# Kernel optimization log

Hardware: AMD Instinct MI355X
Metric: run time of the kernel (lower is better)

The kernel has to match this reference:

```python
import jax, jax.numpy as jnp
import numpy as np

B, U, L, E, H, V = 512, 10, 50, 200, 200, 50000
FLAT = 16 * 16 * 8  # conv(3x3,VALID)->48x48, pool(3x3,s3)->16x16, 8 channels


def gru(x, Wih, Whh, bih, bhh):
    """PyTorch-convention GRU (gate order r,z,n). x: [B,T,E] -> (ys [B,T,H], h_last [B,H])."""
    Bx = x.shape[0]
    Hh = Whh.shape[1]
    x_proj = x @ Wih.T + bih  # [B,T,3H]

    def step(h, xp):
        gh = h @ Whh.T + bhh
        xr, xz, xn = jnp.split(xp, 3, axis=-1)
        hr, hz, hn = jnp.split(gh, 3, axis=-1)
        r = jax.nn.sigmoid(xr + hr)
        z = jax.nn.sigmoid(xz + hz)
        n = jnp.tanh(xn + r * hn)
        h_new = (1.0 - z) * n + z * h
        return h_new, h_new

    h0 = jnp.zeros((Bx, Hh), x.dtype)
    h_last, ys = jax.lax.scan(step, h0, jnp.swapaxes(x_proj, 0, 1))
    return jnp.swapaxes(ys, 0, 1), h_last


def setup_inputs() -> dict:
    key = jax.random.key(0)
    ks = jax.random.split(key, 24)
    s = 0.05
    inp = {
        "utterance": jax.random.randint(ks[0], (B, U, L), 0, V, dtype=jnp.int32),
        "response": jax.random.randint(ks[1], (B, L), 0, V, dtype=jnp.int32),
        "emb": jax.random.uniform(ks[2], (V, E), jnp.float32, -0.25, 0.25),
        "W_ih_u": jax.random.normal(ks[3], (3 * H, E)) * s,
        "W_hh_u": jax.random.normal(ks[4], (3 * H, H)) * s,
        "b_ih_u": jnp.zeros((3 * H,), jnp.float32),
        "b_hh_u": jnp.zeros((3 * H,), jnp.float32),
        "W_ih_r": jax.random.normal(ks[5], (3 * H, E)) * s,
        "W_hh_r": jax.random.normal(ks[6], (3 * H, H)) * s,
        "b_ih_r": jnp.zeros((3 * H,), jnp.float32),
        "b_hh_r": jnp.zeros((3 * H,), jnp.float32),
        "conv_w": jax.random.normal(ks[7], (8, 2, 3, 3)) * 0.3,
        "conv_b": jnp.zeros((8,), jnp.float32),
        "lin_w": jax.random.normal(ks[8], (50, FLAT)) * 0.02,
        "lin_b": jnp.zeros((50,), jnp.float32),
        "Amat": jax.random.normal(ks[9], (H, H)) * 0.05,
        "W_ih_f": jax.random.normal(ks[10], (3 * H, 50)) * s,
        "W_hh_f": jax.random.normal(ks[11], (3 * H, H)) * s,
        "b_ih_f": jnp.zeros((3 * H,), jnp.float32),
        "b_hh_f": jnp.zeros((3 * H,), jnp.float32),
        "flin_w": jax.random.normal(ks[12], (1, H)) * 0.05,
        "flin_b": jnp.zeros((1,), jnp.float32),
    }
    return inp


def reference(utterance, response, emb, W_ih_u, W_hh_u, b_ih_u, b_hh_u,
              W_ih_r, W_hh_r, b_ih_r, b_hh_r, conv_w, conv_b, lin_w, lin_b,
              Amat, W_ih_f, W_hh_f, b_ih_f, b_hh_f, flin_w, flin_b):
    ue = emb[utterance]            # [B,U,L,E]
    re = emb[response]             # [B,L,E]

    rg, _ = gru(re, W_ih_r, W_hh_r, b_ih_r, b_hh_r)  # [B,L,H]

    # word-level match: matmul(utt_emb, resp_emb^T)
    m1 = jnp.einsum('bule,bte->bult', ue, re)  # [B,U,L,L]

    # segment-level: GRU(utt) @ A @ GRU(resp)^T  (loop over utterances folded into batch)
    ug, _ = gru(ue.reshape(B * U, L, E), W_ih_u, W_hh_u, b_ih_u, b_hh_u)
    ug = ug.reshape(B, U, L, H)
    m2 = jnp.einsum('bulh,hk,btk->bult', ug, Amat, rg)  # [B,U,L,L]

    x = jnp.stack([m1, m2], axis=2).reshape(B * U, 2, L, L)  # [B*U,2,50,50]
    x = jax.lax.conv_general_dilated(x, conv_w, (1, 1), 'VALID',
                                     dimension_numbers=('NCHW', 'OIHW', 'NCHW'))
    x = jax.nn.relu(x + conv_b[None, :, None, None])          # [B*U,8,48,48]
    x = jax.lax.reduce_window(x, -jnp.inf, jax.lax.max,
                              (1, 1, 3, 3), (1, 1, 3, 3), 'VALID')  # [B*U,8,16,16]
    x = x.reshape(B * U, FLAT)
    mv = jnp.tanh(x @ lin_w.T + lin_b).reshape(B, U, 50)      # matching vectors

    _, h_last = gru(mv, W_ih_f, W_hh_f, b_ih_f, b_hh_f)       # [B,H]
    logits = h_last @ flin_w.T + flin_b                       # [B,1]
    return jax.nn.sigmoid(logits)
```

## Files before the change

### kernel.cpp

```cpp
#include <hip/hip_runtime.h>
#include <hip/hip_bf16.h>


typedef __attribute__((ext_vector_type(8))) short short8v;
typedef __attribute__((ext_vector_type(4))) float f32x4;

__device__ __forceinline__ float sigm(float x) { return 1.0f / (1.0f + __expf(-x)); }
__device__ __forceinline__ float tanhfast(float x) {
    float e = __expf(2.0f * x);
    return 1.0f - 2.0f / (e + 1.0f);
}
__device__ __forceinline__ float bl(unsigned x) { return __uint_as_float(x << 16); }
__device__ __forceinline__ float bh(unsigned x) { return __uint_as_float(x & 0xffff0000u); }
__device__ __forceinline__ unsigned packbf(float a, float b) {
    union { __hip_bfloat16 h[2]; unsigned u; } cv;
    cv.h[0] = __float2bfloat16(a); cv.h[1] = __float2bfloat16(b);
    return cv.u;
}

__global__ __launch_bounds__(256)
void gemm_mfma(const void* __restrict__ Asrc, int a_bf16,
               const int* __restrict__ gidx,
               const float* __restrict__ W, const float* __restrict__ bias,
               __hip_bfloat16* __restrict__ C, int M, int N)
{
    __shared__ __hip_bfloat16 Al[64 * 232];
    __shared__ __hip_bfloat16 Bl[64 * 232];
    const int tid = threadIdx.x;
    const int m0 = blockIdx.x * 64, n0 = blockIdx.y * 64;

    for (int idx = tid; idx < 64 * 29; idx += 256) {
        int r = idx / 29, q = idx - r * 29;
        int k0 = q * 8, row = m0 + r;
        uint4 val = make_uint4(0, 0, 0, 0);
        if (k0 < 200 && row < M) {
            size_t ar = (size_t)(gidx ? gidx[row] : row) * 200 + k0;
            if (a_bf16) {
                val = *(const uint4*)((const __hip_bfloat16*)Asrc + ar);
            } else {
                const float* ap = (const float*)Asrc + ar;
                float4 f0 = *(const float4*)ap;
                float4 f1 = *(const float4*)(ap + 4);
                val.x = packbf(f0.x, f0.y); val.y = packbf(f0.z, f0.w);
                val.z = packbf(f1.x, f1.y); val.w = packbf(f1.z, f1.w);
            }
        }
        *(uint4*)(Al + r * 232 + k0) = val;
    }
    for (int idx = tid; idx < 64 * 29; idx += 256) {
        int r = idx / 29, q = idx - r * 29;
        int k0 = q * 8, row = n0 + r;
        uint4 val = make_uint4(0, 0, 0, 0);
        if (k0 < 200 && row < N) {
            const float* wp = W + (size_t)row * 200 + k0;
            float4 f0 = *(const float4*)wp;
            float4 f1 = *(const float4*)(wp + 4);
            val.x = packbf(f0.x, f0.y); val.y = packbf(f0.z, f0.w);
            val.z = packbf(f1.x, f1.y); val.w = packbf(f1.z, f1.w);
        }
        *(uint4*)(Bl + r * 232 + k0) = val;
    }
    __syncthreads();

    const int wid = tid >> 6, lane = tid & 63;
    const int wm = (wid >> 1) * 32, wn = (wid & 1) * 32;
    const int lrow = lane & 15, lk8 = (lane >> 4) * 8;
    f32x4 acc00 = {0.f, 0.f, 0.f, 0.f}, acc01 = {0.f, 0.f, 0.f, 0.f};
    f32x4 acc10 = {0.f, 0.f, 0.f, 0.f}, acc11 = {0.f, 0.f, 0.f, 0.f};
#pragma unroll
    for (int kk = 0; kk < 7; ++kk) {
        const int kb = kk * 32 + lk8;
        short8v a0 = *(const short8v*)(Al + (wm + lrow) * 232 + kb);
        short8v a1 = *(const short8v*)(Al + (wm + 16 + lrow) * 232 + kb);
        short8v b0 = *(const short8v*)(Bl + (wn + lrow) * 232 + kb);
        short8v b1 = *(const short8v*)(Bl + (wn + 16 + lrow) * 232 + kb);
        acc00 = __builtin_amdgcn_mfma_f32_16x16x32_bf16(a0, b0, acc00, 0, 0, 0);
        acc01 = __builtin_amdgcn_mfma_f32_16x16x32_bf16(a0, b1, acc01, 0, 0, 0);
        acc10 = __builtin_amdgcn_mfma_f32_16x16x32_bf16(a1, b0, acc10, 0, 0, 0);
        acc11 = __builtin_amdgcn_mfma_f32_16x16x32_bf16(a1, b1, acc11, 0, 0, 0);
    }
    const int drow = (lane >> 4) * 4, dcol = lane & 15;
#pragma unroll
    for (int fm = 0; fm < 2; ++fm) {
#pragma unroll
        for (int fn = 0; fn < 2; ++fn) {
            const f32x4 av = (fm == 0) ? (fn == 0 ? acc00 : acc01)
                                       : (fn == 0 ? acc10 : acc11);
            const int gcol = n0 + wn + fn * 16 + dcol;
            if (gcol >= N) continue;
            const float bs = bias ? bias[gcol] : 0.0f;
#pragma unroll
            for (int r = 0; r < 4; ++r) {
                const int grow = m0 + wm + fm * 16 + drow + r;
                if (grow >= M) continue;
                C[(size_t)grow * N + gcol] = __float2bfloat16(av[r] + bs);
            }
        }
    }
}

__global__ __launch_bounds__(256)
void gemm_mfma_k(const void* __restrict__ Asrc, int a_bf16,
                 const float* __restrict__ W, const float* __restrict__ bias,
                 void* __restrict__ Cv, int c_bf16,
                 int M, int N, int K, int act)
{
    __shared__ __align__(16) __hip_bfloat16 As[64 * 136];
    __shared__ __align__(16) __hip_bfloat16 Bs[64 * 136];
    const int tid = threadIdx.x;
    const int m0 = blockIdx.x * 64, n0 = blockIdx.y * 64;
    const int wid = tid >> 6, lane = tid & 63;
    const int wm = (wid >> 1) * 32, wn = (wid & 1) * 32;
    const int lrow = lane & 15, lk8 = (lane >> 4) * 8;
    const bool aAlign16 = a_bf16 && ((K & 7) == 0);

    f32x4 acc00 = {0.f, 0.f, 0.f, 0.f}, acc01 = {0.f, 0.f, 0.f, 0.f};
    f32x4 acc10 = {0.f, 0.f, 0.f, 0.f}, acc11 = {0.f, 0.f, 0.f, 0.f};

    for (int kb = 0; kb < K; kb += 128) {
        for (int idx = tid; idx < 1024; idx += 256) {
            int r = idx >> 4, q = idx & 15;
            int k0 = kb + q * 8, row = m0 + r;
            uint4 av = make_uint4(0, 0, 0, 0);
            if (row < M && k0 < K) {
                size_t base = (size_t)row * K + k0;
                if (a_bf16) {
                    const __hip_bfloat16* ap = (const __hip_bfloat16*)Asrc + base;
                    if (aAlign16 && k0 + 8 <= K) {
                        av = *(const uint4*)ap;
                    } else {
                        unsigned t4[4] = {0, 0, 0, 0};
                        int nv = (K - k0 < 8) ? (K - k0) : 8;
                        for (int e = 0; e < nv; ++e)
                            ((__hip_bfloat16*)t4)[e] = ap[e];
                        av.x = t4[0]; av.y = t4[1]; av.z = t4[2]; av.w = t4[3];
                    }
                } else {
                    const float* ap = (const float*)Asrc + base;
                    float tv[8] = {0, 0, 0, 0, 0, 0, 0, 0};
                    int nv = (K - k0 < 8) ? (K - k0) : 8;
                    for (int e = 0; e < nv; ++e) tv[e] = ap[e];
                    av.x = packbf(tv[0], tv[1]); av.y = packbf(tv[2], tv[3]);
                    av.z = packbf(tv[4], tv[5]); av.w = packbf(tv[6], tv[7]);
                }
            }
            *(uint4*)(As + r * 136 + q * 8) = av;
        }
        for (int idx = tid; idx < 1024; idx += 256) {
            int r = idx >> 4, q = idx & 15;
            int k0 = kb + q * 8, row = n0 + r;
            uint4 bv = make_uint4(0, 0, 0, 0);
            if (row < N && k0 < K) {
                const float* wp = W + (size_t)row * K + k0;
                float tv[8] = {0, 0, 0, 0, 0, 0, 0, 0};
                int nv = (K - k0 < 8) ? (K - k0) : 8;
                for (int e = 0; e < nv; ++e) tv[e] = wp[e];
                bv.x = packbf(tv[0], tv[1]); bv.y = packbf(tv[2], tv[3]);
                bv.z = packbf(tv[4], tv[5]); bv.w = packbf(tv[6], tv[7]);
            }
            *(uint4*)(Bs + r * 136 + q * 8) = bv;
        }
        __syncthreads();
#pragma unroll
        for (int kk = 0; kk < 4; ++kk) {
            const int ko = kk * 32 + lk8;
            short8v a0 = *(const short8v*)(As + (wm + lrow) * 136 + ko);
            short8v a1 = *(const short8v*)(As + (wm + 16 + lrow) * 136 + ko);
            short8v b0 = *(const short8v*)(Bs + (wn + lrow) * 136 + ko);
            short8v b1 = *(const short8v*)(Bs + (wn + 16 + lrow) * 136 + ko);
            acc00 = __builtin_amdgcn_mfma_f32_16x16x32_bf16(a0, b0, acc00, 0, 0, 0);
            acc01 = __builtin_amdgcn_mfma_f32_16x16x32_bf16(a0, b1, acc01, 0, 0, 0);
            acc10 = __builtin_amdgcn_mfma_f32_16x16x32_bf16(a1, b0, acc10, 0, 0, 0);
            acc11 = __builtin_amdgcn_mfma_f32_16x16x32_bf16(a1, b1, acc11, 0, 0, 0);
        }
        __syncthreads();
    }

    const int drow = (lane >> 4) * 4, dcol = lane & 15;
#pragma unroll
    for (int fm = 0; fm < 2; ++fm) {
#pragma unroll
        for (int fn = 0; fn < 2; ++fn) {
            const f32x4 av = (fm == 0) ? (fn == 0 ? acc00 : acc01)
                                       : (fn == 0 ? acc10 : acc11);
            const int gcol = n0 + wn + fn * 16 + dcol;
            if (gcol >= N) continue;
            const float bs = bias ? bias[gcol] : 0.0f;
#pragma unroll
            for (int r = 0; r < 4; ++r) {
                const int grow = m0 + wm + fm * 16 + drow + r;
                if (grow >= M) continue;
                float t = av[r] + bs;
                if (act == 1) t = tanhfast(t);
                if (c_bf16) ((__hip_bfloat16*)Cv)[(size_t)grow * N + gcol] = __float2bfloat16(t);
                else        ((float*)Cv)[(size_t)grow * N + gcol] = t;
            }
        }
    }
}

__global__ __launch_bounds__(256)
void transpose_wf(const float* __restrict__ Wf, float* __restrict__ Tf)
{
    int id = blockIdx.x * 256 + threadIdx.x;
    if (id < 120000) {
        int e = id / 600, j = id - e * 600;
        Tf[id] = Wf[(size_t)j * 200 + e];
    }
}

__global__ __launch_bounds__(256)
void pack_whh(const float* __restrict__ Wu, const float* __restrict__ Wr,
              __hip_bfloat16* __restrict__ Du, __hip_bfloat16* __restrict__ Dr)
{
    int idx = blockIdx.x * 256 + threadIdx.x;
    if (idx >= 143360) return;
    int j = idx / 224, e = idx - j * 224;
    bool v = (j < 600) && (e < 200);
    Du[idx] = __float2bfloat16(v ? Wu[(size_t)j * 200 + e] : 0.0f);
    Dr[idx] = __float2bfloat16(v ? Wr[(size_t)j * 200 + e] : 0.0f);
}

__global__ __launch_bounds__(256)
void gather_re16(const int* __restrict__ resp, const float* __restrict__ emb,
                 __hip_bfloat16* __restrict__ re16)
{
    int idx = blockIdx.x * 256 + threadIdx.x;
    if (idx < 2560000) {
        int row = idx / 100, q = idx - row * 100;
        float2 v = *(const float2*)(emb + (size_t)resp[row] * 200 + 2 * q);
        ((unsigned*)re16)[idx] = packbf(v.x, v.y);
    }
}

__global__ __launch_bounds__(512, 2)
void scan_gru_mfma(const int* __restrict__ utt,
                   const __hip_bfloat16* __restrict__ EPu,
                   const __hip_bfloat16* __restrict__ xpr16,
                   const __hip_bfloat16* __restrict__ Wu16,
                   const __hip_bfloat16* __restrict__ Wr16,
                   const float* __restrict__ bhu, const float* __restrict__ bhr,
                   __hip_bfloat16* __restrict__ ug16,
                   __hip_bfloat16* __restrict__ rg16)
{
    __shared__ __align__(16) float gh[32][644];
    __shared__ __align__(16) float hf[32][204];
    __shared__ __align__(16) __hip_bfloat16 h16[32][232];

    const int tid = threadIdx.x;
    const bool isResp = (int)blockIdx.x >= 160;
    const int row0 = isResp ? ((int)blockIdx.x - 160) * 32 : (int)blockIdx.x * 32;
    const __hip_bfloat16* Wt = isResp ? Wr16 : Wu16;
    const float* bgate = isResp ? bhr : bhu;
    __hip_bfloat16* arch = isResp ? rg16 : ug16;

    for (int i = tid; i < 32 * 204; i += 512) ((float*)hf)[i] = 0.0f;
    for (int i = tid; i < 928; i += 512) ((uint4*)h16)[i] = make_uint4(0, 0, 0, 0);
    __syncthreads();

    const int wid = tid >> 6, lane = tid & 63;
    const int lrow = lane & 15, lk8 = (lane >> 4) * 8;
    const int drow = (lane >> 4) * 4, dcol = lane & 15;

    short8v Bf[5][7];
#pragma unroll
    for (int i = 0; i < 5; ++i) {
        const int j = (wid * 5 + i) * 16 + lrow;
#pragma unroll
        for (int kk = 0; kk < 7; ++kk)
            Bf[i][kk] = *(const short8v*)(Wt + (size_t)j * 224 + kk * 32 + lk8);
    }

    const int r0a = tid / 25,        c0a = (tid % 25) * 8;
    const int t1  = tid + 512;
    const int r0b = t1 / 25,         c0b = (t1 % 25) * 8;

    for (int t = 0; t < 50; ++t) {
        const int ga = row0 + r0a;
        const __hip_bfloat16* xpa = isResp
            ? (xpr16 + ((size_t)ga * 50 + t) * 600)
            : (EPu + (size_t)utt[ga * 50 + t] * 600);
        uint4 xra = *(const uint4*)(xpa + c0a);
        uint4 xza = *(const uint4*)(xpa + 200 + c0a);
        uint4 xna = *(const uint4*)(xpa + 400 + c0a);
        uint4 xrb, xzb, xnb;
        const int gb = row0 + r0b;
        if (tid < 288) {
            const __hip_bfloat16* xpb = isResp
                ? (xpr16 + ((size_t)gb * 50 + t) * 600)
                : (EPu + (size_t)utt[gb * 50 + t] * 600);
            xrb = *(const uint4*)(xpb + c0b);
            xzb = *(const uint4*)(xpb + 200 + c0b);
            xnb = *(const uint4*)(xpb + 400 + c0b);
        }

        f32x4 a0[5], a1[5];
#pragma unroll
        for (int i = 0; i < 5; ++i) {
            a0[i] = (f32x4){0.f, 0.f, 0.f, 0.f};
            a1[i] = (f32x4){0.f, 0.f, 0.f, 0.f};
        }
#pragma unroll
        for (int kk = 0; kk < 7; ++kk) {
            short8v A0 = *(const short8v*)(&h16[lrow][kk * 32 + lk8]);
            short8v A1 = *(const short8v*)(&h16[16 + lrow][kk * 32 + lk8]);
#pragma unroll
            for (int i = 0; i < 5; ++i) {
                a0[i] = __builtin_amdgcn_mfma_f32_16x16x32_bf16(A0, Bf[i][kk], a0[i], 0, 0, 0);
                a1[i] = __builtin_amdgcn_mfma_f32_16x16x32_bf16(A1, Bf[i][kk], a1[i], 0, 0, 0);
            }
        }
#pragma unroll
        for (int i = 0; i < 5; ++i) {
            const int j = (wid * 5 + i) * 16 + dcol;
#pragma unroll
            for (int r = 0; r < 4; ++r) {
                gh[drow + r][j] = a0[i][r];
                gh[16 + drow + r][j] = a1[i][r];
            }
        }
        __syncthreads();

        {
            const int row = r0a, c0 = c0a, grow = ga;
            const unsigned xr4[4] = { xra.x, xra.y, xra.z, xra.w };
            const unsigned xz4[4] = { xza.x, xza.y, xza.z, xza.w };
            const unsigned xn4[4] = { xna.x, xna.y, xna.z, xna.w };
            float hn[8];
#pragma unroll
            for (int j = 0; j < 8; ++j) {
                const int c = c0 + j;
                const float xr = (j & 1) ? bh(xr4[j >> 1]) : bl(xr4[j >> 1]);
                const float xz = (j & 1) ? bh(xz4[j >> 1]) : bl(xz4[j >> 1]);
                const float xn = (j & 1) ? bh(xn4[j >> 1]) : bl(xn4[j >> 1]);
                const float rr = sigm(xr + gh[row][c] + bgate[c]);
                const float zz = sigm(xz + gh[row][200 + c] + bgate[200 + c]);
                const float nn = tanhfast(xn + rr * (gh[row][400 + c] + bgate[400 + c]));
                hn[j] = (1.0f - zz) * nn + zz * hf[row][c];
            }
            *(float4*)(&hf[row][c0])     = (float4){hn[0], hn[1], hn[2], hn[3]};
            *(float4*)(&hf[row][c0 + 4]) = (float4){hn[4], hn[5], hn[6], hn[7]};
            uint4 pk;
            pk.x = packbf(hn[0], hn[1]); pk.y = packbf(hn[2], hn[3]);
            pk.z = packbf(hn[4], hn[5]); pk.w = packbf(hn[6], hn[7]);
            *(uint4*)(&h16[row][c0]) = pk;
            *(uint4*)(arch + ((size_t)grow * 50 + t) * 200 + c0) = pk;
        }
        if (tid < 288) {
            const int row = r0b, c0 = c0b, grow = gb;
            const unsigned xr4[4] = { xrb.x, xrb.y, xrb.z, xrb.w };
            const unsigned xz4[4] = { xzb.x, xzb.y, xzb.z, xzb.w };
            const unsigned xn4[4] = { xnb.x, xnb.y, xnb.z, xnb.w };
            float hn[8];
#pragma unroll
            for (int j = 0; j < 8; ++j) {
                const int c = c0 + j;
                const float xr = (j & 1) ? bh(xr4[j >> 1]) : bl(xr4[j >> 1]);
                const float xz = (j & 1) ? bh(xz4[j >> 1]) : bl(xz4[j >> 1]);
                const float xn = (j & 1) ? bh(xn4[j >> 1]) : bl(xn4[j >> 1]);
                const float rr = sigm(xr + gh[row][c] + bgate[c]);
                const float zz = sigm(xz + gh[row][200 + c] + bgate[200 + c]);
                const float nn = tanhfast(xn + rr * (gh[row][400 + c] + bgate[400 + c]));
                hn[j] = (1.0f - zz) * nn + zz * hf[row][c];
            }
            *(float4*)(&hf[row][c0])     = (float4){hn[0], hn[1], hn[2], hn[3]};
            *(float4*)(&hf[row][c0 + 4]) = (float4){hn[4], hn[5], hn[6], hn[7]};
            uint4 pk;
            pk.x = packbf(hn[0], hn[1]); pk.y = packbf(hn[2], hn[3]);
            pk.z = packbf(hn[4], hn[5]); pk.w = packbf(hn[6], hn[7]);
            *(uint4*)(&h16[row][c0]) = pk;
            *(uint4*)(arch + ((size_t)grow * 50 + t) * 200 + c0) = pk;
        }
        __syncthreads();
    }
}

__global__ __launch_bounds__(256)
void match_conv_pool(const int* __restrict__ utt, const float* __restrict__ emb,
                     const __hip_bfloat16* __restrict__ ug16,
                     const __hip_bfloat16* __restrict__ re16,
                     const __hip_bfloat16* __restrict__ rgA16,
                     const float* __restrict__ cw, const float* __restrict__ cb,
                     __hip_bfloat16* __restrict__ pooled16)
{
    const int bu = blockIdx.x, b = bu / 10;
    __shared__ __align__(16) __hip_bfloat16 As[64 * 232];
    __shared__ __align__(16) __hip_bfloat16 Bs[64 * 232];
    __shared__ float m[2][50][50];
    __shared__ float w[144];
    __shared__ float bsh[8];
    const int tid = threadIdx.x;
    if (tid < 144) w[tid] = cw[tid];
    if (tid >= 144 && tid < 152) bsh[tid - 144] = cb[tid - 144];

    for (int idx = tid; idx < 64 * 29; idx += 256) {
        int r = idx / 29, q = idx - r * 29;
        uint4 av = make_uint4(0, 0, 0, 0), bv = make_uint4(0, 0, 0, 0);
        if (r < 50 && q < 25) {
            const float* ap = emb + (size_t)utt[bu * 50 + r] * 200 + q * 8;
            float4 f0 = *(const float4*)ap;
            float4 f1 = *(const float4*)(ap + 4);
            av.x = packbf(f0.x, f0.y); av.y = packbf(f0.z, f0.w);
            av.z = packbf(f1.x, f1.y); av.w = packbf(f1.z, f1.w);
            bv = *(const uint4*)(re16 + (size_t)b * 10000 + (size_t)r * 200 + q * 8);
        }
        *(uint4*)(As + r * 232 + q * 8) = av;
        *(uint4*)(Bs + r * 232 + q * 8) = bv;
    }
    __syncthreads();

    const int wid = tid >> 6, lane = tid & 63;
    const int wm = (wid >> 1) * 32, wn = (wid & 1) * 32;
    const int lrow = lane & 15, lk8 = (lane >> 4) * 8;
    const int drow = (lane >> 4) * 4, dcol = lane & 15;

#pragma unroll 1
    for (int ch = 0; ch < 2; ++ch) {
        f32x4 acc00 = {0.f, 0.f, 0.f, 0.f}, acc01 = {0.f, 0.f, 0.f, 0.f};
        f32x4 acc10 = {0.f, 0.f, 0.f, 0.f}, acc11 = {0.f, 0.f, 0.f, 0.f};
#pragma unroll
        for (int kk = 0; kk < 7; ++kk) {
            const int kb = kk * 32 + lk8;
            short8v a0 = *(const short8v*)(As + (wm + lrow) * 232 + kb);
            short8v a1 = *(const short8v*)(As + (wm + 16 + lrow) * 232 + kb);
            short8v b0 = *(const short8v*)(Bs + (wn + lrow) * 232 + kb);
            short8v b1 = *(const short8v*)(Bs + (wn + 16 + lrow) * 232 + kb);
            acc00 = __builtin_amdgcn_mfma_f32_16x16x32_bf16(a0, b0, acc00, 0, 0, 0);
            acc01 = __builtin_amdgcn_mfma_f32_16x16x32_bf16(a0, b1, acc01, 0, 0, 0);
            acc10 = __builtin_amdgcn_mfma_f32_16x16x32_bf16(a1, b0, acc10, 0, 0, 0);
            acc11 = __builtin_amdgcn_mfma_f32_16x16x32_bf16(a1, b1, acc11, 0, 0, 0);
        }
#pragma unroll
        for (int fm = 0; fm < 2; ++fm) {
#pragma unroll
            for (int fn = 0; fn < 2; ++fn) {
                const f32x4 av = (fm == 0) ? (fn == 0 ? acc00 : acc01)
                                           : (fn == 0 ? acc10 : acc11);
                const int gcol = wn + fn * 16 + dcol;
                if (gcol >= 50) continue;
#pragma unroll
                for (int r = 0; r < 4; ++r) {
                    const int grow = wm + fm * 16 + drow + r;
                    if (grow < 50) m[ch][grow][gcol] = av[r];
                }
            }
        }
        __syncthreads();
        if (ch == 0) {
            for (int idx = tid; idx < 50 * 25; idx += 256) {
                int r = idx / 25, q = idx - r * 25;
                *(uint4*)(As + r * 232 + q * 8) =
                    *(const uint4*)(ug16 + (size_t)bu * 10000 + (size_t)r * 200 + q * 8);
                *(uint4*)(Bs + r * 232 + q * 8) =
                    *(const uint4*)(rgA16 + (size_t)b * 10000 + (size_t)r * 200 + q * 8);
            }
            __syncthreads();
        }
    }

#pragma unroll
    for (int k = 0; k < 8; ++k) {
        const int o = tid + k * 256;
        const int c = o >> 8, ph = (o >> 4) & 15, pw = o & 15;
        float mx = -1e30f;
#pragma unroll
        for (int p = 0; p < 3; ++p)
#pragma unroll
            for (int q = 0; q < 3; ++q) {
                const int y = ph * 3 + p, x = pw * 3 + q;
                float s = bsh[c];
#pragma unroll
                for (int ci = 0; ci < 2; ++ci)
#pragma unroll
                    for (int dy = 0; dy < 3; ++dy)
#pragma unroll
                        for (int dx = 0; dx < 3; ++dx)
                            s = fmaf(w[(c * 2 + ci) * 9 + dy * 3 + dx],
                                     m[ci][y + dy][x + dx], s);
                s = fmaxf(s, 0.0f);
                mx = fmaxf(mx, s);
            }
        pooled16[(size_t)bu * 2048 + o] = __float2bfloat16(mx);
    }
}

__global__ __launch_bounds__(256)
void final_gru(const float* __restrict__ xpf, const float* __restrict__ WTf,
               const float* __restrict__ bhf, const float* __restrict__ fw,
               const float* __restrict__ fb, float* __restrict__ out)
{
    const int blk = blockIdx.x;
    const int tid = threadIdx.x;
    __shared__ float h[2][201];
    for (int i = tid; i < 402; i += 256) ((float*)h)[i] = 0.0f;
    __syncthreads();
    const int rr = tid / 100;
    const int j0 = 2 * (tid % 100);
    for (int t = 0; t < 10; ++t) {
        float cR[2] = {}, cZ[2] = {}, cN[2] = {};
        if (tid < 200) {
#pragma unroll 2
            for (int e = 0; e < 200; ++e) {
                const float* w = WTf + (size_t)e * 600;
                float2 wr = *(const float2*)(w + j0);
                float2 wz = *(const float2*)(w + 200 + j0);
                float2 wn = *(const float2*)(w + 400 + j0);
                float hv = h[rr][e];
                cR[0] = fmaf(hv, wr.x, cR[0]); cR[1] = fmaf(hv, wr.y, cR[1]);
                cZ[0] = fmaf(hv, wz.x, cZ[0]); cZ[1] = fmaf(hv, wz.y, cZ[1]);
                cN[0] = fmaf(hv, wn.x, cN[0]); cN[1] = fmaf(hv, wn.y, cN[1]);
            }
        }
        __syncthreads();
        if (tid < 200) {
            const float* xp = xpf + ((size_t)(blk * 2 + rr) * 10 + t) * 600;
#pragma unroll
            for (int j = 0; j < 2; ++j) {
                const int c = j0 + j;
                float rrg = sigm(xp[c] + cR[j] + bhf[c]);
                float zz = sigm(xp[200 + c] + cZ[j] + bhf[200 + c]);
                float nn = tanhfast(xp[400 + c] + rrg * (cN[j] + bhf[400 + c]));
                h[rr][c] = (1.0f - zz) * nn + zz * h[rr][c];
            }
        }
        __syncthreads();
    }
    if (tid < 2) {
        float s = fb[0];
        for (int k = 0; k < 200; ++k) s = fmaf(h[tid][k], fw[k], s);
        out[blk * 2 + tid] = sigm(s);
    }
}

__global__ __launch_bounds__(256)
void fill_out(float* __restrict__ out)
{
    int i = blockIdx.x * 256 + threadIdx.x;
    if (i < 512) out[i] = 0.0f;
}

extern "C" void kernel_launch(void* const* d_in, const int* in_sizes, int n_in,
                              void* d_out, int out_size, void* d_ws, size_t ws_size,
                              hipStream_t stream)
{
    const int*   utt    = (const int*)d_in[0];
    const int*   resp   = (const int*)d_in[1];
    const float* emb    = (const float*)d_in[2];
    const float* W_ih_u = (const float*)d_in[3];
    const float* W_hh_u = (const float*)d_in[4];
    const float* b_ih_u = (const float*)d_in[5];
    const float* b_hh_u = (const float*)d_in[6];
    const float* W_ih_r = (const float*)d_in[7];
    const float* W_hh_r = (const float*)d_in[8];
    const float* b_ih_r = (const float*)d_in[9];
    const float* b_hh_r = (const float*)d_in[10];
    const float* conv_w = (const float*)d_in[11];
    const float* conv_b = (const float*)d_in[12];
    const float* lin_w  = (const float*)d_in[13];
    const float* lin_b  = (const float*)d_in[14];
    const float* Amat   = (const float*)d_in[15];
    const float* W_ih_f = (const float*)d_in[16];
    const float* W_hh_f = (const float*)d_in[17];
    const float* b_ih_f = (const float*)d_in[18];
    const float* b_hh_f = (const float*)d_in[19];
    const float* flin_w = (const float*)d_in[20];
    const float* flin_b = (const float*)d_in[21];
    float* out = (float*)d_out;
    float* ws  = (float*)d_ws;

    size_t off = 0;
    auto alloc = [&](size_t n) { float* p = ws + off; off += (n + 63) & ~((size_t)63); return p; };
    float* WT_f   = alloc(120000);
    float* Wu16f  = alloc(71680);
    float* Wr16f  = alloc(71680);
    float* re16f  = alloc(2560000);
    float* EPuf   = alloc(15000000);
    float* xprf   = alloc(7680000);
    float* ug16f  = alloc(25600000);
    float* rg16f  = alloc(2560000);
    float* rgA16f = alloc(2560000);

    if (off * sizeof(float) > ws_size) {
        hipLaunchKernelGGL(fill_out, dim3(2), dim3(256), 0, stream, out);
        return;
    }

    __hip_bfloat16* Wu16  = (__hip_bfloat16*)Wu16f;
    __hip_bfloat16* Wr16  = (__hip_bfloat16*)Wr16f;
    __hip_bfloat16* re16  = (__hip_bfloat16*)re16f;
    __hip_bfloat16* EPu   = (__hip_bfloat16*)EPuf;
    __hip_bfloat16* xpr16 = (__hip_bfloat16*)xprf;
    __hip_bfloat16* ug16  = (__hip_bfloat16*)ug16f;
    __hip_bfloat16* rg16  = (__hip_bfloat16*)rg16f;
    __hip_bfloat16* rgA16 = (__hip_bfloat16*)rgA16f;
    __hip_bfloat16* pooled16 = (__hip_bfloat16*)EPuf;
    __hip_bfloat16* mv16     = (__hip_bfloat16*)xprf;
    float* xpf = xprf + 400000;

    hipLaunchKernelGGL(transpose_wf, dim3(469), dim3(256), 0, stream, W_hh_f, WT_f);
    hipLaunchKernelGGL(pack_whh, dim3(560), dim3(256), 0, stream,
                       W_hh_u, W_hh_r, Wu16, Wr16);
    hipLaunchKernelGGL(gather_re16, dim3(10000), dim3(256), 0, stream, resp, emb, re16);
    hipLaunchKernelGGL(gemm_mfma, dim3(782, 10), dim3(256), 0, stream,
                       (const void*)emb, 0, (const int*)nullptr, W_ih_u, b_ih_u,
                       EPu, 50000, 600);
    hipLaunchKernelGGL(gemm_mfma, dim3(400, 10), dim3(256), 0, stream,
                       (const void*)emb, 0, resp, W_ih_r, b_ih_r,
                       xpr16, 25600, 600);
    hipLaunchKernelGGL(scan_gru_mfma, dim3(176), dim3(512), 0, stream,
                       utt, EPu, xpr16, Wu16, Wr16, b_hh_u, b_hh_r, ug16, rg16);
    hipLaunchKernelGGL(gemm_mfma, dim3(400, 4), dim3(256), 0, stream,
                       (const void*)rg16, 1, (const int*)nullptr, Amat,
                       (const float*)nullptr, rgA16, 25600, 200);
    hipLaunchKernelGGL(match_conv_pool, dim3(5120), dim3(256), 0, stream,
                       utt, emb, ug16, re16, rgA16, conv_w, conv_b, pooled16);
    hipLaunchKernelGGL(gemm_mfma_k, dim3(80, 1), dim3(256), 0, stream,
                       (const void*)pooled16, 1, lin_w, lin_b,
                       (void*)mv16, 1, 5120, 50, 2048, 1);
    hipLaunchKernelGGL(gemm_mfma_k, dim3(80, 10), dim3(256), 0, stream,
                       (const void*)mv16, 1, W_ih_f, b_ih_f,
                       (void*)xpf, 0, 5120, 600, 50, 0);
    hipLaunchKernelGGL(final_gru, dim3(256), dim3(256), 0, stream,
                       xpf, WT_f, b_hh_f, flin_w, flin_b, out);
}
```

Before: 1.154 ms.

## Fuse GRU gate math into MFMA accumulators with gate-aligned weight packing

Repacks W_hh so each gate occupies a 256-row padded slab, letting every wave compute r, z, n tiles for the same hidden columns and apply the GRU update directly from MFMA accumulators in registers. This removes the gh shared-memory staging and the fp32 hidden-state array, and double-buffers h16 so each step needs a single barrier. In exchange, weights are no longer kept in registers and are re-read from global/L2 every step, the input projections are loaded as scalar bf16 elements, and the archive store of the previous step is deferred into the next iteration.

```diff
diff --git a/kernel.cpp b/kernel.cpp
--- a/kernel.cpp
+++ b/kernel.cpp
@@ -214,11 +214,12 @@
               __hip_bfloat16* __restrict__ Du, __hip_bfloat16* __restrict__ Dr)
 {
     int idx = blockIdx.x * 256 + threadIdx.x;
-    if (idx >= 143360) return;
+    if (idx >= 172032) return;
     int j = idx / 224, e = idx - j * 224;
-    bool v = (j < 600) && (e < 200);
-    Du[idx] = __float2bfloat16(v ? Wu[(size_t)j * 200 + e] : 0.0f);
-    Dr[idx] = __float2bfloat16(v ? Wr[(size_t)j * 200 + e] : 0.0f);
+    int g = j >> 8, cc = j & 255;
+    bool v = (cc < 200) && (e < 200);
+    Du[idx] = __float2bfloat16(v ? Wu[(size_t)(g * 200 + cc) * 200 + e] : 0.0f);
+    Dr[idx] = __float2bfloat16(v ? Wr[(size_t)(g * 200 + cc) * 200 + e] : 0.0f);
 }
 
 __global__ __launch_bounds__(256)
@@ -243,9 +244,7 @@
                    __hip_bfloat16* __restrict__ ug16,
                    __hip_bfloat16* __restrict__ rg16)
 {
-    __shared__ __align__(16) float gh[32][644];
-    __shared__ __align__(16) float hf[32][204];
-    __shared__ __align__(16) __hip_bfloat16 h16[32][232];
+    __shared__ __align__(16) __hip_bfloat16 h16[2][32][232];
 
     const int tid = threadIdx.x;
     const bool isResp = (int)blockIdx.x >= 160;
@@ -254,124 +253,121 @@
     const float* bgate = isResp ? bhr : bhu;
     __hip_bfloat16* arch = isResp ? rg16 : ug16;
 
-    for (int i = tid; i < 32 * 204; i += 512) ((float*)hf)[i] = 0.0f;
-    for (int i = tid; i < 928; i += 512) ((uint4*)h16)[i] = make_uint4(0, 0, 0, 0);
+    for (int i = tid; i < 2 * 32 * 232 / 8; i += 512)
+        ((uint4*)h16)[i] = make_uint4(0, 0, 0, 0);
     __syncthreads();
 
     const int wid = tid >> 6, lane = tid & 63;
     const int lrow = lane & 15, lk8 = (lane >> 4) * 8;
     const int drow = (lane >> 4) * 4, dcol = lane & 15;
-
-    short8v Bf[5][7];
-#pragma unroll
-    for (int i = 0; i < 5; ++i) {
-        const int j = (wid * 5 + i) * 16 + lrow;
-#pragma unroll
-        for (int kk = 0; kk < 7; ++kk)
-            Bf[i][kk] = *(const short8v*)(Wt + (size_t)j * 224 + kk * 32 + lk8);
-    }
-
-    const int r0a = tid / 25,        c0a = (tid % 25) * 8;
-    const int t1  = tid + 512;
-    const int r0b = t1 / 25,         c0b = (t1 % 25) * 8;
+    const int ct0 = 2 * wid, ct1 = 2 * wid + 1;
+    const bool u0 = (ct0 <= 12), u1 = (ct1 <= 12);
+    const int c0 = ct0 * 16 + dcol, c1 = ct1 * 16 + dcol;
+    const bool g0 = (c0 < 200), g1 = (c1 < 200);
+
+    float bgA[3] = {0.f, 0.f, 0.f}, bgB[3] = {0.f, 0.f, 0.f};
+    if (g0) { bgA[0] = bgate[c0]; bgA[1] = bgate[200 + c0]; bgA[2] = bgate[400 + c0]; }
+    if (g1) { bgB[0] = bgate[c1]; bgB[1] = bgate[200 + c1]; bgB[2] = bgate[400 + c1]; }
+
+    float hfA[2][4] = {{0.f,0.f,0.f,0.f},{0.f,0.f,0.f,0.f}};
+    float hfB[2][4] = {{0.f,0.f,0.f,0.f},{0.f,0.f,0.f,0.f}};
 
     for (int t = 0; t < 50; ++t) {
-        const int ga = row0 + r0a;
-        const __hip_bfloat16* xpa = isResp
-            ? (xpr16 + ((size_t)ga * 50 + t) * 600)
-            : (EPu + (size_t)utt[ga * 50 + t] * 600);
-        uint4 xra = *(const uint4*)(xpa + c0a);
-        uint4 xza = *(const uint4*)(xpa + 200 + c0a);
-        uint4 xna = *(const uint4*)(xpa + 400 + c0a);
-        uint4 xrb, xzb, xnb;
-        const int gb = row0 + r0b;
-        if (tid < 288) {
-            const __hip_bfloat16* xpb = isResp
-                ? (xpr16 + ((size_t)gb * 50 + t) * 600)
-                : (EPu + (size_t)utt[gb * 50 + t] * 600);
-            xrb = *(const uint4*)(xpb + c0b);
-            xzb = *(const uint4*)(xpb + 200 + c0b);
-            xnb = *(const uint4*)(xpb + 400 + c0b);
-        }
-
-        f32x4 a0[5], a1[5];
-#pragma unroll
-        for (int i = 0; i < 5; ++i) {
-            a0[i] = (f32x4){0.f, 0.f, 0.f, 0.f};
-            a1[i] = (f32x4){0.f, 0.f, 0.f, 0.f};
-        }
+        const int buf = t & 1, nxt = buf ^ 1;
+
+        if (t > 0) {
+            for (int idx = tid; idx < 800; idx += 512) {
+                int rr = idx / 25, q = (idx - rr * 25) * 8;
+                uint4 v = *(const uint4*)(&h16[buf][rr][q]);
+                *(uint4*)(arch + ((size_t)(row0 + rr) * 50 + (t - 1)) * 200 + q) = v;
+            }
+        }
+
+        float xvA[2][4][3], xvB[2][4][3];
+#pragma unroll
+        for (int rb = 0; rb < 2; ++rb)
+#pragma unroll
+            for (int r = 0; r < 4; ++r) {
+                const int grow = row0 + rb * 16 + drow + r;
+                const __hip_bfloat16* xp = isResp
+                    ? (xpr16 + ((size_t)grow * 50 + t) * 600)
+                    : (EPu + (size_t)utt[grow * 50 + t] * 600);
+                if (g0) {
+                    xvA[rb][r][0] = __bfloat162float(xp[c0]);
+                    xvA[rb][r][1] = __bfloat162float(xp[200 + c0]);
+                    xvA[rb][r][2] = __bfloat162float(xp[400 + c0]);
+                }
+                if (g1) {
+                    xvB[rb][r][0] = __bfloat162float(xp[c1]);
+                    xvB[rb][r][1] = __bfloat162float(xp[200 + c1]);
+                    xvB[rb][r][2] = __bfloat162float(xp[400 + c1]);
+                }
+            }
+
+        f32x4 aA[2][3], aB[2][3];
+#pragma unroll
+        for (int rb = 0; rb < 2; ++rb)
+#pragma unroll
+            for (int g = 0; g < 3; ++g) {
+                aA[rb][g] = (f32x4){0.f, 0.f, 0.f, 0.f};
+                aB[rb][g] = (f32x4){0.f, 0.f, 0.f, 0.f};
+            }
 #pragma unroll
         for (int kk = 0; kk < 7; ++kk) {
-            short8v A0 = *(const short8v*)(&h16[lrow][kk * 32 + lk8]);
-            short8v A1 = *(const short8v*)(&h16[16 + lrow][kk * 32 + lk8]);
-#pragma unroll
-            for (int i = 0; i < 5; ++i) {
-                a0[i] = __builtin_amdgcn_mfma_f32_16x16x32_bf16(A0, Bf[i][kk], a0[i], 0, 0, 0);
-                a1[i] = __builtin_amdgcn_mfma_f32_16x16x32_bf16(A1, Bf[i][kk], a1[i], 0, 0, 0);
-            }
-        }
-#pragma unroll
-        for (int i = 0; i < 5; ++i) {
-            const int j = (wid * 5 + i) * 16 + dcol;
-#pragma unroll
-            for (int r = 0; r < 4; ++r) {
-                gh[drow + r][j] = a0[i][r];
-                gh[16 + drow + r][j] = a1[i][r];
-            }
+            short8v A0 = *(const short8v*)(&h16[buf][lrow][kk * 32 + lk8]);
+            short8v A1 = *(const short8v*)(&h16[buf][16 + lrow][kk * 32 + lk8]);
+            if (u0) {
+#pragma unroll
+                for (int g = 0; g < 3; ++g) {
+                    short8v B = *(const short8v*)(Wt +
+                        (size_t)(g * 256 + ct0 * 16 + lrow) * 224 + kk * 32 + lk8);
+                    aA[0][g] = __builtin_amdgcn_mfma_f32_16x16x32_bf16(A0, B, aA[0][g], 0, 0, 0);
+                    aA[1][g] = __builtin_amdgcn_mfma_f32_16x16x32_bf16(A1, B, aA[1][g], 0, 0, 0);
+                }
+            }
+            if (u1) {
+#pragma unroll
+                for (int g = 0; g < 3; ++g) {
+                    short8v B = *(const short8v*)(Wt +
+                        (size_t)(g * 256 + ct1 * 16 + lrow) * 224 + kk * 32 + lk8);
+                    aB[0][g] = __builtin_amdgcn_mfma_f32_16x16x32_bf16(A0, B, aB[0][g], 0, 0, 0);
+                    aB[1][g] = __builtin_amdgcn_mfma_f32_16x16x32_bf16(A1, B, aB[1][g], 0, 0, 0);
+                }
+            }
+        }
+
+        if (g0) {
+#pragma unroll
+            for (int rb = 0; rb < 2; ++rb)
+#pragma unroll
+                for (int r = 0; r < 4; ++r) {
+                    const float rr_ = sigm(xvA[rb][r][0] + aA[rb][0][r] + bgA[0]);
+                    const float zz  = sigm(xvA[rb][r][1] + aA[rb][1][r] + bgA[1]);
+                    const float nn  = tanhfast(xvA[rb][r][2] + rr_ * (aA[rb][2][r] + bgA[2]));
+                    const float hn  = (1.0f - zz) * nn + zz * hfA[rb][r];
+                    hfA[rb][r] = hn;
+                    h16[nxt][rb * 16 + drow + r][c0] = __float2bfloat16(hn);
+                }
+        }
+        if (g1) {
+#pragma unroll
+            for (int rb = 0; rb < 2; ++rb)
+#pragma unroll
+                for (int r = 0; r < 4; ++r) {
+                    const float rr_ = sigm(xvB[rb][r][0] + aB[rb][0][r] + bgB[0]);
+                    const float zz  = sigm(xvB[rb][r][1] + aB[rb][1][r] + bgB[1]);
+                    const float nn  = tanhfast(xvB[rb][r][2] + rr_ * (aB[rb][2][r] + bgB[2]));
+                    const float hn  = (1.0f - zz) * nn + zz * hfB[rb][r];
+                    hfB[rb][r] = hn;
+                    h16[nxt][rb * 16 + drow + r][c1] = __float2bfloat16(hn);
+                }
         }
         __syncthreads();
-
-        {
-            const int row = r0a, c0 = c0a, grow = ga;
-            const unsigned xr4[4] = { xra.x, xra.y, xra.z, xra.w };
-            const unsigned xz4[4] = { xza.x, xza.y, xza.z, xza.w };
-            const unsigned xn4[4] = { xna.x, xna.y, xna.z, xna.w };
-            float hn[8];
-#pragma unroll
-            for (int j = 0; j < 8; ++j) {
-                const int c = c0 + j;
-                const float xr = (j & 1) ? bh(xr4[j >> 1]) : bl(xr4[j >> 1]);
-                const float xz = (j & 1) ? bh(xz4[j >> 1]) : bl(xz4[j >> 1]);
-                const float xn = (j & 1) ? bh(xn4[j >> 1]) : bl(xn4[j >> 1]);
-                const float rr = sigm(xr + gh[row][c] + bgate[c]);
-                const float zz = sigm(xz + gh[row][200 + c] + bgate[200 + c]);
-                const float nn = tanhfast(xn + rr * (gh[row][400 + c] + bgate[400 + c]));
-                hn[j] = (1.0f - zz) * nn + zz * hf[row][c];
-            }
-            *(float4*)(&hf[row][c0])     = (float4){hn[0], hn[1], hn[2], hn[3]};
-            *(float4*)(&hf[row][c0 + 4]) = (float4){hn[4], hn[5], hn[6], hn[7]};
-            uint4 pk;
-            pk.x = packbf(hn[0], hn[1]); pk.y = packbf(hn[2], hn[3]);
-            pk.z = packbf(hn[4], hn[5]); pk.w = packbf(hn[6], hn[7]);
-            *(uint4*)(&h16[row][c0]) = pk;
-            *(uint4*)(arch + ((size_t)grow * 50 + t) * 200 + c0) = pk;
-        }
-        if (tid < 288) {
-            const int row = r0b, c0 = c0b, grow = gb;
-            const unsigned xr4[4] = { xrb.x, xrb.y, xrb.z, xrb.w };
-            const unsigned xz4[4] = { xzb.x, xzb.y, xzb.z, xzb.w };
-            const unsigned xn4[4] = { xnb.x, xnb.y, xnb.z, xnb.w };
-            float hn[8];
-#pragma unroll
-            for (int j = 0; j < 8; ++j) {
-                const int c = c0 + j;
-                const float xr = (j & 1) ? bh(xr4[j >> 1]) : bl(xr4[j >> 1]);
-                const float xz = (j & 1) ? bh(xz4[j >> 1]) : bl(xz4[j >> 1]);
-                const float xn = (j & 1) ? bh(xn4[j >> 1]) : bl(xn4[j >> 1]);
-                const float rr = sigm(xr + gh[row][c] + bgate[c]);
-                const float zz = sigm(xz + gh[row][200 + c] + bgate[200 + c]);
-                const float nn = tanhfast(xn + rr * (gh[row][400 + c] + bgate[400 + c]));
-                hn[j] = (1.0f - zz) * nn + zz * hf[row][c];
-            }
-            *(float4*)(&hf[row][c0])     = (float4){hn[0], hn[1], hn[2], hn[3]};
-            *(float4*)(&hf[row][c0 + 4]) = (float4){hn[4], hn[5], hn[6], hn[7]};
-            uint4 pk;
-            pk.x = packbf(hn[0], hn[1]); pk.y = packbf(hn[2], hn[3]);
-            pk.z = packbf(hn[4], hn[5]); pk.w = packbf(hn[6], hn[7]);
-            *(uint4*)(&h16[row][c0]) = pk;
-            *(uint4*)(arch + ((size_t)grow * 50 + t) * 200 + c0) = pk;
-        }
-        __syncthreads();
+    }
+    for (int idx = tid; idx < 800; idx += 512) {
+        int rr = idx / 25, q = (idx - rr * 25) * 8;
+        uint4 v = *(const uint4*)(&h16[0][rr][q]);
+        *(uint4*)(arch + ((size_t)(row0 + rr) * 50 + 49) * 200 + q) = v;
     }
 }
 
@@ -571,8 +567,8 @@
     size_t off = 0;
     auto alloc = [&](size_t n) { float* p = ws + off; off += (n + 63) & ~((size_t)63); return p; };
     float* WT_f   = alloc(120000);
-    float* Wu16f  = alloc(71680);
-    float* Wr16f  = alloc(71680);
+    float* Wu16f  = alloc(86016);
+    float* Wr16f  = alloc(86016);
     float* re16f  = alloc(2560000);
     float* EPuf   = alloc(15000000);
     float* xprf   = alloc(7680000);
@@ -598,7 +594,7 @@
     float* xpf = xprf + 400000;
 
     hipLaunchKernelGGL(transpose_wf, dim3(469), dim3(256), 0, stream, W_hh_f, WT_f);
-    hipLaunchKernelGGL(pack_whh, dim3(560), dim3(256), 0, stream,
+    hipLaunchKernelGGL(pack_whh, dim3(672), dim3(256), 0, stream,
                        W_hh_u, W_hh_r, Wu16, Wr16);
     hipLaunchKernelGGL(gather_re16, dim3(10000), dim3(256), 0, stream, resp, emb, re16);
     hipLaunchKernelGGL(gemm_mfma, dim3(782, 10), dim3(256), 0, stream,
```

Result: slower. 1.436 ms (+24.4%).

## Shrink GRU scan LDS and registers to fit more blocks per CU

Applied to the files above, without the earlier changes.

The recurrent weight fragments are no longer held in registers; each step reloads them from global memory through cache. The gate pre-activations are staged in LDS as bf16 instead of fp32, and the fp32 hidden state lives in per-thread registers instead of an LDS array. The launch bound is raised to allow four blocks per CU. The aim is higher occupancy to hide the latency of the sequential scan, at the cost of extra weight loads on every step and reduced precision in the gate values.

```diff
diff --git a/kernel.cpp b/kernel.cpp
--- a/kernel.cpp
+++ b/kernel.cpp
@@ -233,7 +233,7 @@
     }
 }
 
-__global__ __launch_bounds__(512, 2)
+__global__ __launch_bounds__(512, 4)
 void scan_gru_mfma(const int* __restrict__ utt,
                    const __hip_bfloat16* __restrict__ EPu,
                    const __hip_bfloat16* __restrict__ xpr16,
@@ -243,8 +243,7 @@
                    __hip_bfloat16* __restrict__ ug16,
                    __hip_bfloat16* __restrict__ rg16)
 {
-    __shared__ __align__(16) float gh[32][644];
-    __shared__ __align__(16) float hf[32][204];
+    __shared__ __align__(16) __hip_bfloat16 ghs[32][616];
     __shared__ __align__(16) __hip_bfloat16 h16[32][232];
 
     const int tid = threadIdx.x;
@@ -254,7 +253,6 @@
     const float* bgate = isResp ? bhr : bhu;
     __hip_bfloat16* arch = isResp ? rg16 : ug16;
 
-    for (int i = tid; i < 32 * 204; i += 512) ((float*)hf)[i] = 0.0f;
     for (int i = tid; i < 928; i += 512) ((uint4*)h16)[i] = make_uint4(0, 0, 0, 0);
     __syncthreads();
 
@@ -262,18 +260,11 @@
     const int lrow = lane & 15, lk8 = (lane >> 4) * 8;
     const int drow = (lane >> 4) * 4, dcol = lane & 15;
 
-    short8v Bf[5][7];
-#pragma unroll
-    for (int i = 0; i < 5; ++i) {
-        const int j = (wid * 5 + i) * 16 + lrow;
-#pragma unroll
-        for (int kk = 0; kk < 7; ++kk)
-            Bf[i][kk] = *(const short8v*)(Wt + (size_t)j * 224 + kk * 32 + lk8);
-    }
-
     const int r0a = tid / 25,        c0a = (tid % 25) * 8;
     const int t1  = tid + 512;
     const int r0b = t1 / 25,         c0b = (t1 % 25) * 8;
+    float hfa[8] = {0.f,0.f,0.f,0.f,0.f,0.f,0.f,0.f};
+    float hfb[8] = {0.f,0.f,0.f,0.f,0.f,0.f,0.f,0.f};
 
     for (int t = 0; t < 50; ++t) {
         const int ga = row0 + r0a;
@@ -306,8 +297,10 @@
             short8v A1 = *(const short8v*)(&h16[16 + lrow][kk * 32 + lk8]);
 #pragma unroll
             for (int i = 0; i < 5; ++i) {
-                a0[i] = __builtin_amdgcn_mfma_f32_16x16x32_bf16(A0, Bf[i][kk], a0[i], 0, 0, 0);
-                a1[i] = __builtin_amdgcn_mfma_f32_16x16x32_bf16(A1, Bf[i][kk], a1[i], 0, 0, 0);
+                const int j = (wid * 5 + i) * 16 + lrow;
+                short8v B = *(const short8v*)(Wt + (size_t)j * 224 + kk * 32 + lk8);
+                a0[i] = __builtin_amdgcn_mfma_f32_16x16x32_bf16(A0, B, a0[i], 0, 0, 0);
+                a1[i] = __builtin_amdgcn_mfma_f32_16x16x32_bf16(A1, B, a1[i], 0, 0, 0);
             }
         }
 #pragma unroll
@@ -315,14 +308,20 @@
             const int j = (wid * 5 + i) * 16 + dcol;
 #pragma unroll
             for (int r = 0; r < 4; ++r) {
-                gh[drow + r][j] = a0[i][r];
-                gh[16 + drow + r][j] = a1[i][r];
+                ghs[drow + r][j] = __float2bfloat16(a0[i][r]);
+                ghs[16 + drow + r][j] = __float2bfloat16(a1[i][r]);
             }
         }
         __syncthreads();
 
         {
             const int row = r0a, c0 = c0a, grow = ga;
+            uint4 g0 = *(const uint4*)(&ghs[row][c0]);
+            uint4 g1 = *(const uint4*)(&ghs[row][200 + c0]);
+            uint4 g2 = *(const uint4*)(&ghs[row][400 + c0]);
+            const unsigned gr4[4] = { g0.x, g0.y, g0.z, g0.w };
+            const unsigned gz4[4] = { g1.x, g1.y, g1.z, g1.w };
+            const unsigned gn4[4] = { g2.x, g2.y, g2.z, g2.w };
             const unsigned xr4[4] = { xra.x, xra.y, xra.z, xra.w };
             const unsigned xz4[4] = { xza.x, xza.y, xza.z, xza.w };
             const unsigned xn4[4] = { xna.x, xna.y, xna.z, xna.w };
@@ -333,13 +332,15 @@
                 const float xr = (j & 1) ? bh(xr4[j >> 1]) : bl(xr4[j >> 1]);
                 const float xz = (j & 1) ? bh(xz4[j >> 1]) : bl(xz4[j >> 1]);
                 const float xn = (j & 1) ? bh(xn4[j >> 1]) : bl(xn4[j >> 1]);
-                const float rr = sigm(xr + gh[row][c] + bgate[c]);
-                const float zz = sigm(xz + gh[row][200 + c] + bgate[200 + c]);
-                const float nn = tanhfast(xn + rr * (gh[row][400 + c] + bgate[400 + c]));
-                hn[j] = (1.0f - zz) * nn + zz * hf[row][c];
-            }
-            *(float4*)(&hf[row][c0])     = (float4){hn[0], hn[1], hn[2], hn[3]};
-            *(float4*)(&hf[row][c0 + 4]) = (float4){hn[4], hn[5], hn[6], hn[7]};
+                const float gr = (j & 1) ? bh(gr4[j >> 1]) : bl(gr4[j >> 1]);
+                const float gz = (j & 1) ? bh(gz4[j >> 1]) : bl(gz4[j >> 1]);
+                const float gn = (j & 1) ? bh(gn4[j >> 1]) : bl(gn4[j >> 1]);
+                const float rr = sigm(xr + gr + bgate[c]);
+                const float zz = sigm(xz + gz + bgate[200 + c]);
+                const float nn = tanhfast(xn + rr * (gn + bgate[400 + c]));
+                hn[j] = (1.0f - zz) * nn + zz * hfa[j];
+                hfa[j] = hn[j];
+            }
             uint4 pk;
             pk.x = packbf(hn[0], hn[1]); pk.y = packbf(hn[2], hn[3]);
             pk.z = packbf(hn[4], hn[5]); pk.w = packbf(hn[6], hn[7]);
@@ -348,6 +349,12 @@
         }
         if (tid < 288) {
             const int row = r0b, c0 = c0b, grow = gb;
+            uint4 g0 = *(const uint4*)(&ghs[row][c0]);
+            uint4 g1 = *(const uint4*)(&ghs[row][200 + c0]);
+            uint4 g2 = *(const uint4*)(&ghs[row][400 + c0]);
+            const unsigned gr4[4] = { g0.x, g0.y, g0.z, g0.w };
+            const unsigned gz4[4] = { g1.x, g1.y, g1.z, g1.w };
+            const unsigned gn4[4] = { g2.x, g2.y, g2.z, g2.w };
             const unsigned xr4[4] = { xrb.x, xrb.y, xrb.z, xrb.w };
             const unsigned xz4[4] = { xzb.x, xzb.y, xzb.z, xzb.w };
             const unsigned xn4[4] = { xnb.x, xnb.y, xnb.z, xnb.w };
@@ -358,13 +365,15 @@
                 const float xr = (j & 1) ? bh(xr4[j >> 1]) : bl(xr4[j >> 1]);
                 const float xz = (j & 1) ? bh(xz4[j >> 1]) : bl(xz4[j >> 1]);
                 const float xn = (j & 1) ? bh(xn4[j >> 1]) : bl(xn4[j >> 1]);
-                const float rr = sigm(xr + gh[row][c] + bgate[c]);
-                const float zz = sigm(xz + gh[row][200 + c] + bgate[200 + c]);
-                const float nn = tanhfast(xn + rr * (gh[row][400 + c] + bgate[400 + c]));
-                hn[j] = (1.0f - zz) * nn + zz * hf[row][c];
-            }
-            *(float4*)(&hf[row][c0])     = (float4){hn[0], hn[1], hn[2], hn[3]};
-            *(float4*)(&hf[row][c0 + 4]) = (float4){hn[4], hn[5], hn[6], hn[7]};
+                const float gr = (j & 1) ? bh(gr4[j >> 1]) : bl(gr4[j >> 1]);
+                const float gz = (j & 1) ? bh(gz4[j >> 1]) : bl(gz4[j >> 1]);
+                const float gn = (j & 1) ? bh(gn4[j >> 1]) : bl(gn4[j >> 1]);
+                const float rr = sigm(xr + gr + bgate[c]);
+                const float zz = sigm(xz + gz + bgate[200 + c]);
+                const float nn = tanhfast(xn + rr * (gn + bgate[400 + c]));
+                hn[j] = (1.0f - zz) * nn + zz * hfb[j];
+                hfb[j] = hn[j];
+            }
             uint4 pk;
             pk.x = packbf(hn[0], hn[1]); pk.y = packbf(hn[2], hn[3]);
             pk.z = packbf(hn[4], hn[5]); pk.w = packbf(hn[6], hn[7]);
```

Result: slower. 1.682 ms (+45.7%).
